# Kernel optimization log

Hardware: AMD Instinct MI355X
Metric: run time of the kernel (lower is better)

Reference implementation:

```python
import jax, jax.numpy as jnp
import numpy as np

B, IMG, IND, E, FF = 64, 1024, 64, 4, 16
LN_EPS = 1e-5


def _layernorm(x, g, b):
    m = x.mean(-1, keepdims=True)
    v = ((x - m) ** 2).mean(-1, keepdims=True)
    return (x - m) / jnp.sqrt(v + LN_EPS) * g + b


def _encoder_layer(x, qkv_w, qkv_b, o_w, o_b, ln1_g, ln1_b,
                   ff1_w, ff1_b, ff2_w, ff2_b, ln2_g, ln2_b):
    # Post-norm TransformerEncoderLayer (nhead=1, relu, dropout inactive at eval)
    qkv = x @ qkv_w + qkv_b                      # [B,S,3E]
    q, k, v = jnp.split(qkv, 3, axis=-1)
    scores = jnp.einsum('bsd,btd->bst', q, k) / jnp.sqrt(jnp.float32(E))
    a = jax.nn.softmax(scores, axis=-1)
    attn = jnp.einsum('bst,btd->bsd', a, v) @ o_w + o_b
    x = _layernorm(x + attn, ln1_g, ln1_b)
    ff = jax.nn.relu(x @ ff1_w + ff1_b) @ ff2_w + ff2_b
    x = _layernorm(x + ff, ln2_g, ln2_b)
    return x


def setup_inputs() -> dict:
    ks = iter(jax.random.split(jax.random.key(0), 64))

    def nrm(shape, s=0.1):
        return jax.random.normal(next(ks), shape, jnp.float32) * s

    inp = {
        'image_embeds': nrm((B, IMG, 1), 1.0),
        'indicator_embeds': nrm((B, 1, IND), 1.0),
        'w_in1': nrm((1, E)), 'b_in1': nrm((E,)),
        'w_in2': nrm((1, E)), 'b_in2': nrm((E,)),
        'w_out1': nrm((E, 1)), 'b_out1': nrm((1,)),
        'w_out2': nrm((E, 1)), 'b_out2': nrm((1,)),
    }
    for p in ('t1', 't2'):
        inp[f'{p}_qkv_w'] = nrm((E, 3 * E)); inp[f'{p}_qkv_b'] = nrm((3 * E,))
        inp[f'{p}_o_w'] = nrm((E, E)); inp[f'{p}_o_b'] = nrm((E,))
        inp[f'{p}_ln1_g'] = jnp.ones((E,), jnp.float32); inp[f'{p}_ln1_b'] = jnp.zeros((E,), jnp.float32)
        inp[f'{p}_ff1_w'] = nrm((E, FF)); inp[f'{p}_ff1_b'] = nrm((FF,))
        inp[f'{p}_ff2_w'] = nrm((FF, E)); inp[f'{p}_ff2_b'] = nrm((E,))
        inp[f'{p}_ln2_g'] = jnp.ones((E,), jnp.float32); inp[f'{p}_ln2_b'] = jnp.zeros((E,), jnp.float32)
    inp['w_cls'] = nrm((IMG + IND, 3))
    inp['b_cls'] = nrm((3,))
    return inp


def reference(image_embeds, indicator_embeds,
              w_in1, b_in1, w_in2, b_in2, w_out1, b_out1, w_out2, b_out2,
              t1_qkv_w, t1_qkv_b, t1_o_w, t1_o_b, t1_ln1_g, t1_ln1_b,
              t1_ff1_w, t1_ff1_b, t1_ff2_w, t1_ff2_b, t1_ln2_g, t1_ln2_b,
              t2_qkv_w, t2_qkv_b, t2_o_w, t2_o_b, t2_ln1_g, t2_ln1_b,
              t2_ff1_w, t2_ff1_b, t2_ff2_w, t2_ff2_b, t2_ln2_g, t2_ln2_b,
              w_cls, b_cls):
    ind = jnp.swapaxes(indicator_embeds, 1, 2)   # [B, IND, 1]
    img = image_embeds @ w_in1 + b_in1           # [B, IMG, E]
    img = _encoder_layer(img, t1_qkv_w, t1_qkv_b, t1_o_w, t1_o_b,
                         t1_ln1_g, t1_ln1_b, t1_ff1_w, t1_ff1_b,
                         t1_ff2_w, t1_ff2_b, t1_ln2_g, t1_ln2_b)
    img = img @ w_out1 + b_out1                  # [B, IMG, 1]
    ind = ind @ w_in2 + b_in2                    # [B, IND, E]
    ind = _encoder_layer(ind, t2_qkv_w, t2_qkv_b, t2_o_w, t2_o_b,
                         t2_ln1_g, t2_ln1_b, t2_ff1_w, t2_ff1_b,
                         t2_ff2_w, t2_ff2_b, t2_ln2_g, t2_ln2_b)
    ind = ind @ w_out2 + b_out2                  # [B, IND, 1]
    x = jnp.concatenate((img, ind), axis=1)[..., 0]  # [B, IMG+IND]
    x = x @ w_cls + b_cls                        # [B, 3]
    return jax.nn.softmax(x, axis=-1)
```

## Files before the change

### kernel.cpp

```cpp
#include <hip/hip_runtime.h>

#define B_    64
#define IMG_  1024
#define IND_  64
#define NTHR  256
#define NBLK_IMG (B_ * 4)
#define NBLK  (NBLK_IMG + B_)

enum {
  W_IN = 0, B_IN = 4, QKV_W = 8, QKV_B = 56, O_W = 68, O_B = 84,
  LN1G = 88, LN1B = 92, FF1W = 96, FF1B = 160, FF2W = 176, FF2B = 240,
  LN2G = 244, LN2B = 248, W_OUT = 252, B_OUT = 256, WTOT = 257
};

struct KArgs {
  const float* in[36];
  float* pout;
  float* out;
};

__device__ __forceinline__ void stage(float* dst, const float* src, int n, int tid) {
  for (int i = tid; i < n; i += NTHR) dst[i] = src[i];
}

__device__ __forceinline__ double wave_sum_d(double v) {
  v += __shfl_xor(v, 1);  v += __shfl_xor(v, 2);  v += __shfl_xor(v, 4);
  v += __shfl_xor(v, 8);  v += __shfl_xor(v, 16); v += __shfl_xor(v, 32);
  return v;
}

__global__ __launch_bounds__(NTHR) void enc_rows(KArgs A) {
  const int blk = blockIdx.x;
  const int tid = threadIdx.x;
  const bool is_img = blk < NBLK_IMG;

  __shared__ float w[WTOT];
  __shared__ float iv[IMG_];
  __shared__ double mws[4][13];
  __shared__ float red[4][3];

  int batch, row0, rows, S, tb;
  const float* xin;
  if (is_img) {
    batch = blk >> 2; row0 = (blk & 3) << 8; rows = 256; S = IMG_;
    xin = A.in[0] + batch * IMG_; tb = 10;
  } else {
    batch = blk - NBLK_IMG; row0 = 0; rows = IND_; S = IND_;
    xin = A.in[1] + batch * IND_; tb = 22;
  }

  stage(w + W_IN,  A.in[is_img ? 2 : 4], 4,  tid);
  stage(w + B_IN,  A.in[is_img ? 3 : 5], 4,  tid);
  stage(w + W_OUT, A.in[is_img ? 6 : 8], 4,  tid);
  stage(w + B_OUT, A.in[is_img ? 7 : 9], 1,  tid);
  stage(w + QKV_W, A.in[tb + 0], 48, tid);
  stage(w + QKV_B, A.in[tb + 1], 12, tid);
  stage(w + O_W,   A.in[tb + 2], 16, tid);
  stage(w + O_B,   A.in[tb + 3], 4,  tid);
  stage(w + LN1G,  A.in[tb + 4], 4,  tid);
  stage(w + LN1B,  A.in[tb + 5], 4,  tid);
  stage(w + FF1W,  A.in[tb + 6], 64, tid);
  stage(w + FF1B,  A.in[tb + 7], 16, tid);
  stage(w + FF2W,  A.in[tb + 8], 64, tid);
  stage(w + FF2B,  A.in[tb + 9], 4,  tid);
  stage(w + LN2G,  A.in[tb + 10], 4, tid);
  stage(w + LN2B,  A.in[tb + 11], 4, tid);
  for (int i = tid; i < S; i += NTHR) iv[i] = xin[i];
  __syncthreads();

  double m[13];
#pragma unroll
  for (int k = 0; k < 13; k++) m[k] = 0.0;
  for (int i = tid; i < S; i += NTHR) {
    const double x = (double)iv[i];
    double px = x;
#pragma unroll
    for (int k = 0; k < 13; k++) { m[k] += px; px *= x; }
  }
#pragma unroll
  for (int k = 0; k < 13; k++) m[k] = wave_sum_d(m[k]);
  if ((tid & 63) == 0) {
    const int wv = tid >> 6;
#pragma unroll
    for (int k = 0; k < 13; k++) mws[wv][k] = m[k];
  }
  __syncthreads();
  float Mf[14];
  Mf[0] = (float)S;
#pragma unroll
  for (int k = 0; k < 13; k++)
    Mf[k + 1] = (float)(mws[0][k] + mws[1][k] + mws[2][k] + mws[3][k]);

  float qd[4], qb[4], kd[4], vd[4], vb[4];
#pragma unroll
  for (int j = 0; j < 4; j++) {
    float a0 = 0.f, a1 = 0.f, a2 = 0.f, b0 = 0.f, b2 = 0.f;
#pragma unroll
    for (int e = 0; e < 4; e++) {
      const float we = w[W_IN + e], be = w[B_IN + e];
      a0 += we * w[QKV_W + e * 12 + j];      b0 += be * w[QKV_W + e * 12 + j];
      a1 += we * w[QKV_W + e * 12 + 4 + j];
      a2 += we * w[QKV_W + e * 12 + 8 + j];  b2 += be * w[QKV_W + e * 12 + 8 + j];
    }
    qd[j] = a0; qb[j] = b0 + w[QKV_B + j];
    kd[j] = a1;
    vd[j] = a2; vb[j] = b2 + w[QKV_B + 8 + j];
  }
  float c1 = 0.f, c0 = 0.f;
#pragma unroll
  for (int j = 0; j < 4; j++) { c1 += qd[j] * kd[j]; c0 += qb[j] * kd[j]; }
  float HB[4], HC[4];
#pragma unroll
  for (int j = 0; j < 4; j++) {
    float s1 = 0.f, s2 = 0.f;
#pragma unroll
    for (int f = 0; f < 4; f++) {
      s1 += vd[f] * w[O_W + f * 4 + j];
      s2 += vb[f] * w[O_W + f * 4 + j];
    }
    HB[j] = s1; HC[j] = w[B_IN + j] + s2 + w[O_B + j];
  }

  const bool active = tid < rows;
  const int row = row0 + (active ? tid : 0);
  const float ivr = iv[row];
  const float a = 0.5f * (c1 * ivr + c0);

  float t = 1.f, S0 = Mf[0], S1 = Mf[1];
#pragma unroll
  for (int k = 1; k <= 12; k++) {
    t *= a * (1.0f / (float)k);
    S0 = fmaf(t, Mf[k], S0);
    S1 = fmaf(t, Mf[k + 1], S1);
  }
  const float rho = S1 / S0;

  float h[4];
#pragma unroll
  for (int j = 0; j < 4; j++) h[j] = w[W_IN + j] * ivr + HB[j] * rho + HC[j];
  {
    const float mn = 0.25f * (h[0] + h[1] + h[2] + h[3]);
    float v = 0.f;
#pragma unroll
    for (int j = 0; j < 4; j++) { const float d = h[j] - mn; v += d * d; }
    const float rs = rsqrtf(v * 0.25f + 1e-5f);
#pragma unroll
    for (int j = 0; j < 4; j++) h[j] = (h[j] - mn) * rs * w[LN1G + j] + w[LN1B + j];
  }
  float f2[4] = {w[FF2B + 0], w[FF2B + 1], w[FF2B + 2], w[FF2B + 3]};
#pragma unroll
  for (int tt = 0; tt < 16; tt++) {
    float u = w[FF1B + tt];
#pragma unroll
    for (int j = 0; j < 4; j++) u += h[j] * w[FF1W + j * 16 + tt];
    u = fmaxf(u, 0.f);
#pragma unroll
    for (int j = 0; j < 4; j++) f2[j] += u * w[FF2W + tt * 4 + j];
  }
  float h2[4];
#pragma unroll
  for (int j = 0; j < 4; j++) h2[j] = h[j] + f2[j];
  {
    const float mn = 0.25f * (h2[0] + h2[1] + h2[2] + h2[3]);
    float v = 0.f;
#pragma unroll
    for (int j = 0; j < 4; j++) { const float d = h2[j] - mn; v += d * d; }
    const float rs = rsqrtf(v * 0.25f + 1e-5f);
#pragma unroll
    for (int j = 0; j < 4; j++) h2[j] = (h2[j] - mn) * rs * w[LN2G + j] + w[LN2B + j];
  }
  float outv = w[B_OUT];
#pragma unroll
  for (int j = 0; j < 4; j++) outv += h2[j] * w[W_OUT + j];

  float p0 = 0.f, p1 = 0.f, p2 = 0.f;
  if (active) {
    const int g = is_img ? row : (IMG_ + row);
    const float* wc = A.in[34] + 3 * g;
    p0 = outv * wc[0]; p1 = outv * wc[1]; p2 = outv * wc[2];
  }
#pragma unroll
  for (int msk = 1; msk < 64; msk <<= 1) {
    p0 += __shfl_xor(p0, msk); p1 += __shfl_xor(p1, msk); p2 += __shfl_xor(p2, msk);
  }
  if ((tid & 63) == 0) {
    const int wv = tid >> 6;
    red[wv][0] = p0; red[wv][1] = p1; red[wv][2] = p2;
  }
  __syncthreads();
  if (tid == 0) {
    A.pout[blk * 3 + 0] = red[0][0] + red[1][0] + red[2][0] + red[3][0];
    A.pout[blk * 3 + 1] = red[0][1] + red[1][1] + red[2][1] + red[3][1];
    A.pout[blk * 3 + 2] = red[0][2] + red[1][2] + red[2][2] + red[3][2];
  }
}

__global__ __launch_bounds__(64) void finalize(const float* __restrict__ pout,
                                               const float* __restrict__ b_cls,
                                               float* __restrict__ out) {
  const int b = threadIdx.x;
  float z[3];
#pragma unroll
  for (int c = 0; c < 3; c++) {
    float s = b_cls[c];
    for (int i = 0; i < 4; i++) s += pout[(4 * b + i) * 3 + c];
    s += pout[(NBLK_IMG + b) * 3 + c];
    z[c] = s;
  }
  const float mx = fmaxf(z[0], fmaxf(z[1], z[2]));
  const float e0 = __expf(z[0] - mx), e1 = __expf(z[1] - mx), e2 = __expf(z[2] - mx);
  const float rs = 1.f / (e0 + e1 + e2);
  out[b * 3 + 0] = e0 * rs;
  out[b * 3 + 1] = e1 * rs;
  out[b * 3 + 2] = e2 * rs;
}

extern "C" void kernel_launch(void* const* d_in, const int* in_sizes, int n_in,
                              void* d_out, int out_size, void* d_ws, size_t ws_size,
                              hipStream_t stream) {
  KArgs A;
  for (int i = 0; i < 36; i++) A.in[i] = (const float*)d_in[i];
  A.pout = (float*)d_ws;
  A.out  = (float*)d_out;

  enc_rows<<<NBLK, NTHR, 0, stream>>>(A);
  finalize<<<1, 64, 0, stream>>>(A.pout, A.in[35], (float*)d_out);
}
```

Baseline: 134.2 us.

## Fuse encoder rows and softmax finalize into one per-batch kernel

Replaces the two-kernel scheme (320 blocks of 256 threads plus a finalize kernel) with a single kernel of 64 blocks of 1024 threads, one per batch. Each block computes the image moments once instead of redundantly in four blocks, handles the indicator rows in the first wave, and does the classifier softmax in-block. This removes the second launch and the workspace round-trip, at the cost of fewer, larger blocks and more serial work in wave 0.

```diff
diff --git a/kernel.cpp b/kernel.cpp
--- a/kernel.cpp
+++ b/kernel.cpp
@@ -3,9 +3,7 @@
 #define B_    64
 #define IMG_  1024
 #define IND_  64
-#define NTHR  256
-#define NBLK_IMG (B_ * 4)
-#define NBLK  (NBLK_IMG + B_)
+#define NTHR  1024
 
 enum {
   W_IN = 0, B_IN = 4, QKV_W = 8, QKV_B = 56, O_W = 68, O_B = 84,
@@ -15,7 +13,6 @@
 
 struct KArgs {
   const float* in[36];
-  float* pout;
   float* out;
 };
 
@@ -29,68 +26,8 @@
   return v;
 }
 
-__global__ __launch_bounds__(NTHR) void enc_rows(KArgs A) {
-  const int blk = blockIdx.x;
-  const int tid = threadIdx.x;
-  const bool is_img = blk < NBLK_IMG;
-
-  __shared__ float w[WTOT];
-  __shared__ float iv[IMG_];
-  __shared__ double mws[4][13];
-  __shared__ float red[4][3];
-
-  int batch, row0, rows, S, tb;
-  const float* xin;
-  if (is_img) {
-    batch = blk >> 2; row0 = (blk & 3) << 8; rows = 256; S = IMG_;
-    xin = A.in[0] + batch * IMG_; tb = 10;
-  } else {
-    batch = blk - NBLK_IMG; row0 = 0; rows = IND_; S = IND_;
-    xin = A.in[1] + batch * IND_; tb = 22;
-  }
-
-  stage(w + W_IN,  A.in[is_img ? 2 : 4], 4,  tid);
-  stage(w + B_IN,  A.in[is_img ? 3 : 5], 4,  tid);
-  stage(w + W_OUT, A.in[is_img ? 6 : 8], 4,  tid);
-  stage(w + B_OUT, A.in[is_img ? 7 : 9], 1,  tid);
-  stage(w + QKV_W, A.in[tb + 0], 48, tid);
-  stage(w + QKV_B, A.in[tb + 1], 12, tid);
-  stage(w + O_W,   A.in[tb + 2], 16, tid);
-  stage(w + O_B,   A.in[tb + 3], 4,  tid);
-  stage(w + LN1G,  A.in[tb + 4], 4,  tid);
-  stage(w + LN1B,  A.in[tb + 5], 4,  tid);
-  stage(w + FF1W,  A.in[tb + 6], 64, tid);
-  stage(w + FF1B,  A.in[tb + 7], 16, tid);
-  stage(w + FF2W,  A.in[tb + 8], 64, tid);
-  stage(w + FF2B,  A.in[tb + 9], 4,  tid);
-  stage(w + LN2G,  A.in[tb + 10], 4, tid);
-  stage(w + LN2B,  A.in[tb + 11], 4, tid);
-  for (int i = tid; i < S; i += NTHR) iv[i] = xin[i];
-  __syncthreads();
-
-  double m[13];
-#pragma unroll
-  for (int k = 0; k < 13; k++) m[k] = 0.0;
-  for (int i = tid; i < S; i += NTHR) {
-    const double x = (double)iv[i];
-    double px = x;
-#pragma unroll
-    for (int k = 0; k < 13; k++) { m[k] += px; px *= x; }
-  }
-#pragma unroll
-  for (int k = 0; k < 13; k++) m[k] = wave_sum_d(m[k]);
-  if ((tid & 63) == 0) {
-    const int wv = tid >> 6;
-#pragma unroll
-    for (int k = 0; k < 13; k++) mws[wv][k] = m[k];
-  }
-  __syncthreads();
-  float Mf[14];
-  Mf[0] = (float)S;
-#pragma unroll
-  for (int k = 0; k < 13; k++)
-    Mf[k + 1] = (float)(mws[0][k] + mws[1][k] + mws[2][k] + mws[3][k]);
-
+__device__ __forceinline__ float row_tail(const float* __restrict__ w,
+                                          float ivr, const float* __restrict__ Mf) {
   float qd[4], qb[4], kd[4], vd[4], vb[4];
 #pragma unroll
   for (int j = 0; j < 4; j++) {
@@ -121,11 +58,7 @@
     HB[j] = s1; HC[j] = w[B_IN + j] + s2 + w[O_B + j];
   }
 
-  const bool active = tid < rows;
-  const int row = row0 + (active ? tid : 0);
-  const float ivr = iv[row];
   const float a = 0.5f * (c1 * ivr + c0);
-
   float t = 1.f, S0 = Mf[0], S1 = Mf[1];
 #pragma unroll
   for (int k = 1; k <= 12; k++) {
@@ -172,13 +105,96 @@
   float outv = w[B_OUT];
 #pragma unroll
   for (int j = 0; j < 4; j++) outv += h2[j] * w[W_OUT + j];
-
-  float p0 = 0.f, p1 = 0.f, p2 = 0.f;
-  if (active) {
-    const int g = is_img ? row : (IMG_ + row);
-    const float* wc = A.in[34] + 3 * g;
-    p0 = outv * wc[0]; p1 = outv * wc[1]; p2 = outv * wc[2];
-  }
+  return outv;
+}
+
+__global__ __launch_bounds__(NTHR) void fused(KArgs A) {
+  const int b = blockIdx.x;
+  const int tid = threadIdx.x;
+
+  __shared__ float w1[WTOT], w2[WTOT];
+  __shared__ float ivI[IMG_];
+  __shared__ float ivN[IND_];
+  __shared__ double mws[16][13];
+  __shared__ double mfin[13];
+  __shared__ float red[16][3];
+
+  stage(w1 + W_IN,  A.in[2], 4, tid);  stage(w1 + B_IN,  A.in[3], 4, tid);
+  stage(w1 + W_OUT, A.in[6], 4, tid);  stage(w1 + B_OUT, A.in[7], 1, tid);
+  stage(w2 + W_IN,  A.in[4], 4, tid);  stage(w2 + B_IN,  A.in[5], 4, tid);
+  stage(w2 + W_OUT, A.in[8], 4, tid);  stage(w2 + B_OUT, A.in[9], 1, tid);
+#pragma unroll
+  for (int s = 0; s < 2; s++) {
+    float* w = s ? w2 : w1;
+    const int tb = s ? 22 : 10;
+    stage(w + QKV_W, A.in[tb + 0], 48, tid);
+    stage(w + QKV_B, A.in[tb + 1], 12, tid);
+    stage(w + O_W,   A.in[tb + 2], 16, tid);
+    stage(w + O_B,   A.in[tb + 3], 4,  tid);
+    stage(w + LN1G,  A.in[tb + 4], 4,  tid);
+    stage(w + LN1B,  A.in[tb + 5], 4,  tid);
+    stage(w + FF1W,  A.in[tb + 6], 64, tid);
+    stage(w + FF1B,  A.in[tb + 7], 16, tid);
+    stage(w + FF2W,  A.in[tb + 8], 64, tid);
+    stage(w + FF2B,  A.in[tb + 9], 4,  tid);
+    stage(w + LN2G,  A.in[tb + 10], 4, tid);
+    stage(w + LN2B,  A.in[tb + 11], 4, tid);
+  }
+  for (int i = tid; i < IMG_; i += NTHR) ivI[i] = A.in[0][b * IMG_ + i];
+  for (int i = tid; i < IND_; i += NTHR) ivN[i] = A.in[1][b * IND_ + i];
+  __syncthreads();
+
+  double m[13];
+  {
+    const double x = (double)ivI[tid];
+    double px = x;
+#pragma unroll
+    for (int k = 0; k < 13; k++) { m[k] = px; px *= x; }
+  }
+#pragma unroll
+  for (int k = 0; k < 13; k++) m[k] = wave_sum_d(m[k]);
+  if ((tid & 63) == 0) {
+    const int wv = tid >> 6;
+#pragma unroll
+    for (int k = 0; k < 13; k++) mws[wv][k] = m[k];
+  }
+  __syncthreads();
+  if (tid < 13) {
+    double s = 0.0;
+#pragma unroll
+    for (int wv = 0; wv < 16; wv++) s += mws[wv][tid];
+    mfin[tid] = s;
+  }
+  __syncthreads();
+  float MfI[14];
+  MfI[0] = (float)IMG_;
+#pragma unroll
+  for (int k = 0; k < 13; k++) MfI[k + 1] = (float)mfin[k];
+
+  const float outI = row_tail(w1, ivI[tid], MfI);
+  float p0, p1, p2;
+  {
+    const float* wc = A.in[34] + 3 * tid;
+    p0 = outI * wc[0]; p1 = outI * wc[1]; p2 = outI * wc[2];
+  }
+
+  if (tid < 64) {
+    double mi[13];
+    const double x = (double)ivN[tid];
+    double px = x;
+#pragma unroll
+    for (int k = 0; k < 13; k++) { mi[k] = px; px *= x; }
+#pragma unroll
+    for (int k = 0; k < 13; k++) mi[k] = wave_sum_d(mi[k]);
+    float MfN[14];
+    MfN[0] = (float)IND_;
+#pragma unroll
+    for (int k = 0; k < 13; k++) MfN[k + 1] = (float)mi[k];
+    const float outN = row_tail(w2, ivN[tid], MfN);
+    const float* wc = A.in[34] + 3 * (IMG_ + tid);
+    p0 += outN * wc[0]; p1 += outN * wc[1]; p2 += outN * wc[2];
+  }
+
 #pragma unroll
   for (int msk = 1; msk < 64; msk <<= 1) {
     p0 += __shfl_xor(p0, msk); p1 += __shfl_xor(p1, msk); p2 += __shfl_xor(p2, msk);
@@ -189,30 +205,22 @@
   }
   __syncthreads();
   if (tid == 0) {
-    A.pout[blk * 3 + 0] = red[0][0] + red[1][0] + red[2][0] + red[3][0];
-    A.pout[blk * 3 + 1] = red[0][1] + red[1][1] + red[2][1] + red[3][1];
-    A.pout[blk * 3 + 2] = red[0][2] + red[1][2] + red[2][2] + red[3][2];
-  }
-}
-
-__global__ __launch_bounds__(64) void finalize(const float* __restrict__ pout,
-                                               const float* __restrict__ b_cls,
-                                               float* __restrict__ out) {
-  const int b = threadIdx.x;
-  float z[3];
-#pragma unroll
-  for (int c = 0; c < 3; c++) {
-    float s = b_cls[c];
-    for (int i = 0; i < 4; i++) s += pout[(4 * b + i) * 3 + c];
-    s += pout[(NBLK_IMG + b) * 3 + c];
-    z[c] = s;
-  }
-  const float mx = fmaxf(z[0], fmaxf(z[1], z[2]));
-  const float e0 = __expf(z[0] - mx), e1 = __expf(z[1] - mx), e2 = __expf(z[2] - mx);
-  const float rs = 1.f / (e0 + e1 + e2);
-  out[b * 3 + 0] = e0 * rs;
-  out[b * 3 + 1] = e1 * rs;
-  out[b * 3 + 2] = e2 * rs;
+    const float* bc = A.in[35];
+    float z[3];
+#pragma unroll
+    for (int c = 0; c < 3; c++) {
+      float s = bc[c];
+#pragma unroll
+      for (int wv = 0; wv < 16; wv++) s += red[wv][c];
+      z[c] = s;
+    }
+    const float mx = fmaxf(z[0], fmaxf(z[1], z[2]));
+    const float e0 = __expf(z[0] - mx), e1 = __expf(z[1] - mx), e2 = __expf(z[2] - mx);
+    const float rs = 1.f / (e0 + e1 + e2);
+    A.out[b * 3 + 0] = e0 * rs;
+    A.out[b * 3 + 1] = e1 * rs;
+    A.out[b * 3 + 2] = e2 * rs;
+  }
 }
 
 extern "C" void kernel_launch(void* const* d_in, const int* in_sizes, int n_in,
@@ -220,9 +228,6 @@
                               hipStream_t stream) {
   KArgs A;
   for (int i = 0; i < 36; i++) A.in[i] = (const float*)d_in[i];
-  A.pout = (float*)d_ws;
-  A.out  = (float*)d_out;
-
-  enc_rows<<<NBLK, NTHR, 0, stream>>>(A);
-  finalize<<<1, 64, 0, stream>>>(A.pout, A.in[35], (float*)d_out);
-}
+  A.out = (float*)d_out;
+  fused<<<B_, NTHR, 0, stream>>>(A);
+}
```

Result: slower. 148.1 us (+10.4%).

## Fuse finalize into encoder kernel via cooperative grid sync

Applied to the files above, without the earlier changes.

Merges the per-row encoder kernel and the softmax finalize kernel into one cooperative launch, using a grid-wide sync before blocks 0..63 compute the class softmax. Token values are now loaded directly into registers instead of staged through shared memory, and the per-row tail is moved into a helper. This removes a second kernel launch and the shared-memory staging pass, but adds the cost of a cooperative launch and grid barrier. It also requires all 320 blocks to be co-resident.

```diff
diff --git a/kernel.cpp b/kernel.cpp
--- a/kernel.cpp
+++ b/kernel.cpp
@@ -1,4 +1,7 @@
 #include <hip/hip_runtime.h>
+#include <hip/hip_cooperative_groups.h>
+
+namespace cg = cooperative_groups;
 
 #define B_    64
 #define IMG_  1024
@@ -29,24 +32,103 @@
   return v;
 }
 
-__global__ __launch_bounds__(NTHR) void enc_rows(KArgs A) {
+__device__ __forceinline__ float row_tail(const float* __restrict__ w,
+                                          float ivr, const float* __restrict__ Mf) {
+  float qd[4], qb[4], kd[4], vd[4], vb[4];
+#pragma unroll
+  for (int j = 0; j < 4; j++) {
+    float a0 = 0.f, a1 = 0.f, a2 = 0.f, b0 = 0.f, b2 = 0.f;
+#pragma unroll
+    for (int e = 0; e < 4; e++) {
+      const float we = w[W_IN + e], be = w[B_IN + e];
+      a0 += we * w[QKV_W + e * 12 + j];      b0 += be * w[QKV_W + e * 12 + j];
+      a1 += we * w[QKV_W + e * 12 + 4 + j];
+      a2 += we * w[QKV_W + e * 12 + 8 + j];  b2 += be * w[QKV_W + e * 12 + 8 + j];
+    }
+    qd[j] = a0; qb[j] = b0 + w[QKV_B + j];
+    kd[j] = a1;
+    vd[j] = a2; vb[j] = b2 + w[QKV_B + 8 + j];
+  }
+  float c1 = 0.f, c0 = 0.f;
+#pragma unroll
+  for (int j = 0; j < 4; j++) { c1 += qd[j] * kd[j]; c0 += qb[j] * kd[j]; }
+  float HB[4], HC[4];
+#pragma unroll
+  for (int j = 0; j < 4; j++) {
+    float s1 = 0.f, s2 = 0.f;
+#pragma unroll
+    for (int f = 0; f < 4; f++) {
+      s1 += vd[f] * w[O_W + f * 4 + j];
+      s2 += vb[f] * w[O_W + f * 4 + j];
+    }
+    HB[j] = s1; HC[j] = w[B_IN + j] + s2 + w[O_B + j];
+  }
+
+  const float a = 0.5f * (c1 * ivr + c0);
+  float t = 1.f, S0 = Mf[0], S1 = Mf[1];
+#pragma unroll
+  for (int k = 1; k <= 12; k++) {
+    t *= a * (1.0f / (float)k);
+    S0 = fmaf(t, Mf[k], S0);
+    S1 = fmaf(t, Mf[k + 1], S1);
+  }
+  const float rho = S1 / S0;
+
+  float h[4];
+#pragma unroll
+  for (int j = 0; j < 4; j++) h[j] = w[W_IN + j] * ivr + HB[j] * rho + HC[j];
+  {
+    const float mn = 0.25f * (h[0] + h[1] + h[2] + h[3]);
+    float v = 0.f;
+#pragma unroll
+    for (int j = 0; j < 4; j++) { const float d = h[j] - mn; v += d * d; }
+    const float rs = rsqrtf(v * 0.25f + 1e-5f);
+#pragma unroll
+    for (int j = 0; j < 4; j++) h[j] = (h[j] - mn) * rs * w[LN1G + j] + w[LN1B + j];
+  }
+  float f2[4] = {w[FF2B + 0], w[FF2B + 1], w[FF2B + 2], w[FF2B + 3]};
+#pragma unroll
+  for (int tt = 0; tt < 16; tt++) {
+    float u = w[FF1B + tt];
+#pragma unroll
+    for (int j = 0; j < 4; j++) u += h[j] * w[FF1W + j * 16 + tt];
+    u = fmaxf(u, 0.f);
+#pragma unroll
+    for (int j = 0; j < 4; j++) f2[j] += u * w[FF2W + tt * 4 + j];
+  }
+  float h2[4];
+#pragma unroll
+  for (int j = 0; j < 4; j++) h2[j] = h[j] + f2[j];
+  {
+    const float mn = 0.25f * (h2[0] + h2[1] + h2[2] + h2[3]);
+    float v = 0.f;
+#pragma unroll
+    for (int j = 0; j < 4; j++) { const float d = h2[j] - mn; v += d * d; }
+    const float rs = rsqrtf(v * 0.25f + 1e-5f);
+#pragma unroll
+    for (int j = 0; j < 4; j++) h2[j] = (h2[j] - mn) * rs * w[LN2G + j] + w[LN2B + j];
+  }
+  float outv = w[B_OUT];
+#pragma unroll
+  for (int j = 0; j < 4; j++) outv += h2[j] * w[W_OUT + j];
+  return outv;
+}
+
+__global__ __launch_bounds__(NTHR) void fused(KArgs A) {
   const int blk = blockIdx.x;
   const int tid = threadIdx.x;
   const bool is_img = blk < NBLK_IMG;
 
   __shared__ float w[WTOT];
-  __shared__ float iv[IMG_];
   __shared__ double mws[4][13];
   __shared__ float red[4][3];
 
-  int batch, row0, rows, S, tb;
+  int batch, tb;
   const float* xin;
   if (is_img) {
-    batch = blk >> 2; row0 = (blk & 3) << 8; rows = 256; S = IMG_;
-    xin = A.in[0] + batch * IMG_; tb = 10;
+    batch = blk >> 2; xin = A.in[0] + batch * IMG_; tb = 10;
   } else {
-    batch = blk - NBLK_IMG; row0 = 0; rows = IND_; S = IND_;
-    xin = A.in[1] + batch * IND_; tb = 22;
+    batch = blk - NBLK_IMG; xin = A.in[1] + batch * IND_; tb = 22;
   }
 
   stage(w + W_IN,  A.in[is_img ? 2 : 4], 4,  tid);
@@ -65,14 +147,30 @@
   stage(w + FF2B,  A.in[tb + 9], 4,  tid);
   stage(w + LN2G,  A.in[tb + 10], 4, tid);
   stage(w + LN2B,  A.in[tb + 11], 4, tid);
-  for (int i = tid; i < S; i += NTHR) iv[i] = xin[i];
+
+  float tok[4];
+  if (is_img) {
+#pragma unroll
+    for (int q = 0; q < 4; q++) tok[q] = xin[tid + 256 * q];
+  } else {
+    tok[0] = (tid < IND_) ? xin[tid] : 0.f;
+    tok[1] = tok[2] = tok[3] = 0.f;
+  }
   __syncthreads();
 
   double m[13];
 #pragma unroll
   for (int k = 0; k < 13; k++) m[k] = 0.0;
-  for (int i = tid; i < S; i += NTHR) {
-    const double x = (double)iv[i];
+  if (is_img) {
+#pragma unroll
+    for (int q = 0; q < 4; q++) {
+      const double x = (double)tok[q];
+      double px = x;
+#pragma unroll
+      for (int k = 0; k < 13; k++) { m[k] += px; px *= x; }
+    }
+  } else {
+    const double x = (double)tok[0];
     double px = x;
 #pragma unroll
     for (int k = 0; k < 13; k++) { m[k] += px; px *= x; }
@@ -86,96 +184,18 @@
   }
   __syncthreads();
   float Mf[14];
-  Mf[0] = (float)S;
+  Mf[0] = (float)(is_img ? IMG_ : IND_);
 #pragma unroll
   for (int k = 0; k < 13; k++)
     Mf[k + 1] = (float)(mws[0][k] + mws[1][k] + mws[2][k] + mws[3][k]);
 
-  float qd[4], qb[4], kd[4], vd[4], vb[4];
-#pragma unroll
-  for (int j = 0; j < 4; j++) {
-    float a0 = 0.f, a1 = 0.f, a2 = 0.f, b0 = 0.f, b2 = 0.f;
-#pragma unroll
-    for (int e = 0; e < 4; e++) {
-      const float we = w[W_IN + e], be = w[B_IN + e];
-      a0 += we * w[QKV_W + e * 12 + j];      b0 += be * w[QKV_W + e * 12 + j];
-      a1 += we * w[QKV_W + e * 12 + 4 + j];
-      a2 += we * w[QKV_W + e * 12 + 8 + j];  b2 += be * w[QKV_W + e * 12 + 8 + j];
-    }
-    qd[j] = a0; qb[j] = b0 + w[QKV_B + j];
-    kd[j] = a1;
-    vd[j] = a2; vb[j] = b2 + w[QKV_B + 8 + j];
-  }
-  float c1 = 0.f, c0 = 0.f;
-#pragma unroll
-  for (int j = 0; j < 4; j++) { c1 += qd[j] * kd[j]; c0 += qb[j] * kd[j]; }
-  float HB[4], HC[4];
-#pragma unroll
-  for (int j = 0; j < 4; j++) {
-    float s1 = 0.f, s2 = 0.f;
-#pragma unroll
-    for (int f = 0; f < 4; f++) {
-      s1 += vd[f] * w[O_W + f * 4 + j];
-      s2 += vb[f] * w[O_W + f * 4 + j];
-    }
-    HB[j] = s1; HC[j] = w[B_IN + j] + s2 + w[O_B + j];
-  }
-
-  const bool active = tid < rows;
-  const int row = row0 + (active ? tid : 0);
-  const float ivr = iv[row];
-  const float a = 0.5f * (c1 * ivr + c0);
-
-  float t = 1.f, S0 = Mf[0], S1 = Mf[1];
-#pragma unroll
-  for (int k = 1; k <= 12; k++) {
-    t *= a * (1.0f / (float)k);
-    S0 = fmaf(t, Mf[k], S0);
-    S1 = fmaf(t, Mf[k + 1], S1);
-  }
-  const float rho = S1 / S0;
-
-  float h[4];
-#pragma unroll
-  for (int j = 0; j < 4; j++) h[j] = w[W_IN + j] * ivr + HB[j] * rho + HC[j];
-  {
-    const float mn = 0.25f * (h[0] + h[1] + h[2] + h[3]);
-    float v = 0.f;
-#pragma unroll
-    for (int j = 0; j < 4; j++) { const float d = h[j] - mn; v += d * d; }
-    const float rs = rsqrtf(v * 0.25f + 1e-5f);
-#pragma unroll
-    for (int j = 0; j < 4; j++) h[j] = (h[j] - mn) * rs * w[LN1G + j] + w[LN1B + j];
-  }
-  float f2[4] = {w[FF2B + 0], w[FF2B + 1], w[FF2B + 2], w[FF2B + 3]};
-#pragma unroll
-  for (int tt = 0; tt < 16; tt++) {
-    float u = w[FF1B + tt];
-#pragma unroll
-    for (int j = 0; j < 4; j++) u += h[j] * w[FF1W + j * 16 + tt];
-    u = fmaxf(u, 0.f);
-#pragma unroll
-    for (int j = 0; j < 4; j++) f2[j] += u * w[FF2W + tt * 4 + j];
-  }
-  float h2[4];
-#pragma unroll
-  for (int j = 0; j < 4; j++) h2[j] = h[j] + f2[j];
-  {
-    const float mn = 0.25f * (h2[0] + h2[1] + h2[2] + h2[3]);
-    float v = 0.f;
-#pragma unroll
-    for (int j = 0; j < 4; j++) { const float d = h2[j] - mn; v += d * d; }
-    const float rs = rsqrtf(v * 0.25f + 1e-5f);
-#pragma unroll
-    for (int j = 0; j < 4; j++) h2[j] = (h2[j] - mn) * rs * w[LN2G + j] + w[LN2B + j];
-  }
-  float outv = w[B_OUT];
-#pragma unroll
-  for (int j = 0; j < 4; j++) outv += h2[j] * w[W_OUT + j];
-
+  const bool active = is_img || (tid < IND_);
+  const int q = blk & 3;
+  const float ivr = is_img ? tok[q] : tok[0];
   float p0 = 0.f, p1 = 0.f, p2 = 0.f;
   if (active) {
-    const int g = is_img ? row : (IMG_ + row);
+    const float outv = row_tail(w, ivr, Mf);
+    const int g = is_img ? (q * 256 + tid) : (IMG_ + tid);
     const float* wc = A.in[34] + 3 * g;
     p0 = outv * wc[0]; p1 = outv * wc[1]; p2 = outv * wc[2];
   }
@@ -193,26 +213,28 @@
     A.pout[blk * 3 + 1] = red[0][1] + red[1][1] + red[2][1] + red[3][1];
     A.pout[blk * 3 + 2] = red[0][2] + red[1][2] + red[2][2] + red[3][2];
   }
-}
-
-__global__ __launch_bounds__(64) void finalize(const float* __restrict__ pout,
-                                               const float* __restrict__ b_cls,
-                                               float* __restrict__ out) {
-  const int b = threadIdx.x;
-  float z[3];
-#pragma unroll
-  for (int c = 0; c < 3; c++) {
-    float s = b_cls[c];
-    for (int i = 0; i < 4; i++) s += pout[(4 * b + i) * 3 + c];
-    s += pout[(NBLK_IMG + b) * 3 + c];
-    z[c] = s;
-  }
-  const float mx = fmaxf(z[0], fmaxf(z[1], z[2]));
-  const float e0 = __expf(z[0] - mx), e1 = __expf(z[1] - mx), e2 = __expf(z[2] - mx);
-  const float rs = 1.f / (e0 + e1 + e2);
-  out[b * 3 + 0] = e0 * rs;
-  out[b * 3 + 1] = e1 * rs;
-  out[b * 3 + 2] = e2 * rs;
+
+  __threadfence();
+  cg::this_grid().sync();
+
+  if (blk < B_ && tid == 0) {
+    const float* bc = A.in[35];
+    float z[3];
+#pragma unroll
+    for (int c = 0; c < 3; c++) {
+      float s = bc[c];
+#pragma unroll
+      for (int i = 0; i < 4; i++) s += A.pout[(4 * blk + i) * 3 + c];
+      s += A.pout[(NBLK_IMG + blk) * 3 + c];
+      z[c] = s;
+    }
+    const float mx = fmaxf(z[0], fmaxf(z[1], z[2]));
+    const float e0 = __expf(z[0] - mx), e1 = __expf(z[1] - mx), e2 = __expf(z[2] - mx);
+    const float rs = 1.f / (e0 + e1 + e2);
+    A.out[blk * 3 + 0] = e0 * rs;
+    A.out[blk * 3 + 1] = e1 * rs;
+    A.out[blk * 3 + 2] = e2 * rs;
+  }
 }
 
 extern "C" void kernel_launch(void* const* d_in, const int* in_sizes, int n_in,
@@ -223,6 +245,6 @@
   A.pout = (float*)d_ws;
   A.out  = (float*)d_out;
 
-  enc_rows<<<NBLK, NTHR, 0, stream>>>(A);
-  finalize<<<1, 64, 0, stream>>>(A.pout, A.in[35], (float*)d_out);
-}
+  void* args[] = {(void*)&A};
+  hipLaunchCooperativeKernel((void*)fused, dim3(NBLK), dim3(NTHR), args, 0, stream);
+}
```

Result: slower. 253.4 us (+88.9%).
